# Kernel tuning notes

Measured on AMD Instinct MI355X. Metric: run time of the kernel, lower is better.

Reference implementation:

```python
import jax, jax.numpy as jnp
import numpy as np

ROPE_BASE = 10000.0


def _apply_rope(x, positions):
    # x: [B, S, H, Dh], positions: [S]
    d_head = x.shape[-1]
    half = d_head // 2
    inv_freq = 1.0 / (ROPE_BASE ** (jnp.arange(0, half, dtype=jnp.float32) * 2.0 / d_head))
    angles = positions.astype(jnp.float32)[:, None] * inv_freq[None, :]  # [S, half]
    cos = jnp.cos(angles)[None, :, None, :]  # [1,S,1,half]
    sin = jnp.sin(angles)[None, :, None, :]
    x1, x2 = jnp.split(x, 2, axis=-1)
    return jnp.concatenate([x1 * cos - x2 * sin, x1 * sin + x2 * cos], axis=-1)


def _alibi_slopes(n_heads):
    # standard ALiBi slopes: 2^(-8*(h+1)/n_heads)
    return 2.0 ** (-8.0 * (jnp.arange(1, n_heads + 1, dtype=jnp.float32) / n_heads))


def setup_inputs() -> dict:
    key = jax.random.key(0)
    ks = jax.random.split(key, 5)
    B, S, D = 2, 2048, 2048
    H, KVH, Dh = 16, 4, 128
    std = 0.02
    return {
        "residual": jax.random.normal(ks[0], (B, S, D), dtype=jnp.float32),
        "W_Q": jax.random.normal(ks[1], (H, Dh, D), dtype=jnp.float32) * std,
        "W_K": jax.random.normal(ks[2], (KVH, Dh, D), dtype=jnp.float32) * std,
        "W_V": jax.random.normal(ks[3], (KVH, Dh, D), dtype=jnp.float32) * std,
        "W_O": jax.random.normal(ks[4], (H, Dh, D), dtype=jnp.float32) * std,
        "start_pos": 0,
    }


def reference(residual, W_Q, W_K, W_V, W_O, start_pos):
    B, S, D = residual.shape
    H, Dh, _ = W_Q.shape
    KVH = W_K.shape[0]
    # projections (prefill path: cache=None, total_len == S)
    q = jnp.einsum('bsd,hed->bshe', residual, W_Q)   # [B,S,H,Dh]
    k = jnp.einsum('bsd,hed->bshe', residual, W_K)   # [B,S,KVH,Dh]
    v = jnp.einsum('bsd,hed->bshe', residual, W_V)   # [B,S,KVH,Dh]
    # RoPE
    positions = start_pos + jnp.arange(S)
    q = _apply_rope(q, positions)
    k = _apply_rope(k, positions)
    k_for_cache = k
    v_for_cache = v
    # GQA head repeat
    rep = H // KVH
    k_r = jnp.repeat(k, rep, axis=2)
    v_r = jnp.repeat(v, rep, axis=2)
    # attention scores [B,H,Sq,Sk]
    scores = jnp.einsum('bqhe,bkhe->bhqk', q, k_r) / jnp.sqrt(jnp.float32(Dh))
    # ALiBi bias (sliced rows start_pos:start_pos+S of the total_len x total_len bias)
    slopes = _alibi_slopes(H)  # [H]
    qpos = start_pos + jnp.arange(S)
    kpos = jnp.arange(S)
    bias = -slopes[:, None, None] * (qpos[:, None] - kpos[None, :]).astype(jnp.float32)
    scores = scores + bias[None, :, :, :]
    # causal mask: keep j <= i (tril of ones)
    mask = kpos[None, :] <= qpos[:, None]  # with start_pos=0 this is tril
    scores = jnp.where(mask[None, None, :, :], scores, -jnp.inf)
    pattern = jax.nn.softmax(scores, axis=-1)
    attn = jnp.einsum('bhqk,bkhe->bqhe', pattern, v_r)
    output = jnp.einsum('bqhe,hed->bqd', attn, W_O)
    return output, k_for_cache, v_for_cache
```

## Files before the change

kernel.cpp:

```cpp
#include <hip/hip_runtime.h>


typedef __attribute__((ext_vector_type(8))) short frag8;
typedef __attribute__((ext_vector_type(4))) float facc4;

#define DEVI __device__ __forceinline__

constexpr int Bc  = 2;
constexpr int Sc  = 2048;
constexpr int Dc  = 2048;
constexpr int Hc  = 16;
constexpr int KVHc = 4;
constexpr int Dhc = 128;
constexpr int Mc  = Bc * Sc;
constexpr int NQc = Hc * Dhc;
constexpr int NKVc = KVHc * Dhc;

DEVI unsigned short f2bf(float f) {
  union { float f; unsigned u; } v; v.f = f;
  return (unsigned short)((v.u + 0x7fffu + ((v.u >> 16) & 1u)) >> 16);
}
DEVI float bf2f(unsigned short h) {
  union { unsigned u; float f; } v; v.u = ((unsigned)h) << 16;
  return v.f;
}

DEVI void gload_lds16(const void* g, void* l) {
  __builtin_amdgcn_global_load_lds(
      (const __attribute__((address_space(1))) unsigned int*)g,
      (__attribute__((address_space(3))) unsigned int*)l, 16, 0, 0);
}

DEVI float rowred_max(float x) {
  union { float f; int i; } a, b;
  a.f = x;
  b.i = __builtin_amdgcn_update_dpp(a.i, a.i, 0x128, 0xF, 0xF, false); a.f = fmaxf(a.f, b.f);
  b.i = __builtin_amdgcn_update_dpp(a.i, a.i, 0x124, 0xF, 0xF, false); a.f = fmaxf(a.f, b.f);
  b.i = __builtin_amdgcn_update_dpp(a.i, a.i, 0x122, 0xF, 0xF, false); a.f = fmaxf(a.f, b.f);
  b.i = __builtin_amdgcn_update_dpp(a.i, a.i, 0x121, 0xF, 0xF, false); a.f = fmaxf(a.f, b.f);
  return a.f;
}
DEVI float rowred_sum(float x) {
  union { float f; int i; } a, b;
  a.f = x;
  b.i = __builtin_amdgcn_update_dpp(a.i, a.i, 0x128, 0xF, 0xF, false); a.f += b.f;
  b.i = __builtin_amdgcn_update_dpp(a.i, a.i, 0x124, 0xF, 0xF, false); a.f += b.f;
  b.i = __builtin_amdgcn_update_dpp(a.i, a.i, 0x122, 0xF, 0xF, false); a.f += b.f;
  b.i = __builtin_amdgcn_update_dpp(a.i, a.i, 0x121, 0xF, 0xF, false); a.f += b.f;
  return a.f;
}


__global__ void cvt_all(const float* __restrict__ residual,
                        const float* __restrict__ WQ,
                        const float* __restrict__ WK,
                        const float* __restrict__ WV,
                        const float* __restrict__ WO,
                        unsigned short* __restrict__ rb,
                        unsigned short* __restrict__ wqb,
                        unsigned short* __restrict__ wkvb,
                        unsigned short* __restrict__ wob) {
  __shared__ float tile[64][65];
  int bid = blockIdx.x;
  int t = threadIdx.x;
  if (bid < 14336) {
    const float* src; unsigned short* dst; int off;
    if (bid < 8192)       { src = residual; dst = rb;  off = bid; }
    else if (bid < 12288) { src = WQ; dst = wqb; off = bid - 8192; }
    else if (bid < 13312) { src = WK; dst = wkvb; off = bid - 12288; }
    else                  { src = WV; dst = wkvb + (size_t)NKVc * Dc; off = bid - 13312; }
    int i = (off * 256 + t) * 4;
    float4 v = *(const float4*)(src + i);
    ushort4 o;
    o.x = f2bf(v.x); o.y = f2bf(v.y); o.z = f2bf(v.z); o.w = f2bf(v.w);
    *(ushort4*)(dst + i) = o;
  } else {
    int tb = bid - 14336;
    int r0 = (tb >> 5) * 64;
    int c0 = (tb & 31) * 64;
#pragma unroll
    for (int i = 0; i < 16; ++i) {
      int idx = i * 256 + t; int r = idx >> 6, c = idx & 63;
      tile[r][c] = WO[(size_t)(r0 + r) * Dc + c0 + c];
    }
    __syncthreads();
#pragma unroll
    for (int i = 0; i < 16; ++i) {
      int idx = i * 256 + t; int r = idx >> 6, c = idx & 63;
      wob[(size_t)(c0 + r) * NQc + r0 + c] = f2bf(tile[c][r]);
    }
  }
}


DEVI void stage_tile(const unsigned short* A, const unsigned short* B,
                     unsigned short* Al, unsigned short* Bl,
                     int m0, int n0, int kt, int t, int Kk) {
#pragma unroll
  for (int i = 0; i < 4; ++i) {
    int c = i * 256 + t;
    int row = c >> 3, ch = c & 7;
    int g = ch ^ (row & 7);
    gload_lds16(A + (size_t)(m0 + row) * Kk + kt * 64 + g * 8, Al + c * 8);
  }
#pragma unroll
  for (int i = 0; i < 4; ++i) {
    int c = i * 256 + t;
    int row = c >> 3, ch = c & 7;
    int g = ch ^ (row & 7);
    gload_lds16(B + (size_t)(n0 + row) * Kk + kt * 64 + g * 8, Bl + c * 8);
  }
}

template <int MODE>
__global__ __launch_bounds__(256, 2) void gemm2b(
    const unsigned short* __restrict__ Amat,
    const unsigned short* __restrict__ Bmat,
    float* __restrict__ Cf, float* __restrict__ Cf2,
    unsigned short* __restrict__ Cb, unsigned short* __restrict__ Cb2,
    int Nn, int Kk) {
  __shared__ __align__(16) unsigned short As[2][128 * 64];
  __shared__ __align__(16) unsigned short Bs[2][128 * 64];

  int t = threadIdx.x;
  int lane = t & 63, w = t >> 6;
  int quad = lane >> 4, l16 = lane & 15;
  int l7 = l16 & 7;
  int wm = (w >> 1) * 64, wn = (w & 1) * 64;

  int lin = blockIdx.x + gridDim.x * blockIdx.y;
  int xcd = lin & 7, gg = lin >> 3;
  int ypx = gridDim.y >> 3;
  int ny = xcd * ypx + (gg % ypx);
  int nx = gg / ypx;
  int m0 = nx * 128, n0 = ny * 128;
  const int NT = Kk >> 6;

  auto aoff = [&](int mi, int ks) {
    return (wm + mi * 16 + l16) * 64 + (((ks * 4 + quad) ^ l7) * 8);
  };
  auto boff = [&](int ni, int ks) {
    return (wn + ni * 16 + l16) * 64 + (((ks * 4 + quad) ^ l7) * 8);
  };

  stage_tile(Amat, Bmat, As[0], Bs[0], m0, n0, 0, t, Kk);
  if (NT > 1) stage_tile(Amat, Bmat, As[1], Bs[1], m0, n0, 1, t, Kk);
  if (NT > 1) asm volatile("s_waitcnt vmcnt(8)" ::: "memory");
  else        asm volatile("s_waitcnt vmcnt(0)" ::: "memory");
  __builtin_amdgcn_s_barrier();
  asm volatile("" ::: "memory");

  facc4 acc[4][4] = {};

  for (int kt = 0; kt < NT; ++kt) {
    const int p = kt & 1;
    const unsigned short* Ab = As[p];
    const unsigned short* Bb = Bs[p];
    frag8 aFr[4][2], bFr[4][2];
#pragma unroll
    for (int ks = 0; ks < 2; ++ks) {
#pragma unroll
      for (int mi = 0; mi < 4; ++mi) aFr[mi][ks] = *(const frag8*)&Ab[aoff(mi, ks)];
#pragma unroll
      for (int ni = 0; ni < 4; ++ni) bFr[ni][ks] = *(const frag8*)&Bb[boff(ni, ks)];
    }
    asm volatile("s_waitcnt lgkmcnt(0)" ::: "memory");
    __builtin_amdgcn_s_barrier();
    asm volatile("" ::: "memory");

    if (kt + 2 < NT)
      stage_tile(Amat, Bmat, As[p], Bs[p], m0, n0, kt + 2, t, Kk);

    __builtin_amdgcn_s_setprio(1);
#pragma unroll
    for (int ks = 0; ks < 2; ++ks)
#pragma unroll
      for (int mi = 0; mi < 4; ++mi)
#pragma unroll
        for (int ni = 0; ni < 4; ++ni)
          acc[mi][ni] = __builtin_amdgcn_mfma_f32_16x16x32_bf16(
              aFr[mi][ks], bFr[ni][ks], acc[mi][ni], 0, 0, 0);
    __builtin_amdgcn_s_setprio(0);

    if (kt + 2 < NT) asm volatile("s_waitcnt vmcnt(8)" ::: "memory");
    else             asm volatile("s_waitcnt vmcnt(0)" ::: "memory");
    __builtin_amdgcn_s_barrier();
    asm volatile("" ::: "memory");
  }

#pragma unroll
  for (int mi = 0; mi < 4; ++mi)
#pragma unroll
    for (int ni = 0; ni < 4; ++ni)
#pragma unroll
      for (int i = 0; i < 4; ++i) {
        int row = m0 + wm + mi * 16 + quad * 4 + i;
        int col = n0 + wn + ni * 16 + l16;
        float v = acc[mi][ni][i];
        if (MODE == 0) {
          Cf[(size_t)row * Nn + col] = v;
        } else {
          if (col < NQc) {
            Cb[(size_t)row * NQc + col] = f2bf(v);
          } else if (col < NQc + NKVc) {
            Cf[(size_t)row * NKVc + (col - NQc)] = v;
          } else {
            int nc = col - NQc - NKVc;
            Cf2[(size_t)row * NKVc + nc] = v;
            int b = row >> 11, s = row & (Sc - 1);
            Cb2[((size_t)(b * NKVc + nc)) * Sc + s] = f2bf(v);
          }
        }
      }
}


__global__ void rope_all(unsigned short* qb, float* kf, unsigned short* kb,
                         const int* __restrict__ sp) {
  int idx = blockIdx.x * 256 + threadIdx.x;
  constexpr int NQ = Mc * Hc * 64;
  if (idx < NQ) {
    int e = idx & 63, h = (idx >> 6) & 15, m = idx >> 10;
    int s = m & (Sc - 1);
    float pos = (float)(sp[0] + s);
    float invf = exp2f(-(float)e * 0.20762050593046835f);
    float ang = pos * invf;
    float sn, cs; sincosf(ang, &sn, &cs);
    size_t base = (size_t)m * NQc + h * Dhc + e;
    float x1 = bf2f(qb[base]), x2 = bf2f(qb[base + 64]);
    qb[base]      = f2bf(x1 * cs - x2 * sn);
    qb[base + 64] = f2bf(x1 * sn + x2 * cs);
  } else {
    int j = idx - NQ;
    int e = j & 63, kvh = (j >> 6) & 3, m = j >> 8;
    int s = m & (Sc - 1);
    float pos = (float)(sp[0] + s);
    float invf = exp2f(-(float)e * 0.20762050593046835f);
    float ang = pos * invf;
    float sn, cs; sincosf(ang, &sn, &cs);
    size_t base = (size_t)m * NKVc + kvh * Dhc + e;
    float x1 = kf[base], x2 = kf[base + 64];
    float o1 = x1 * cs - x2 * sn;
    float o2 = x1 * sn + x2 * cs;
    kf[base] = o1; kf[base + 64] = o2;
    kb[base] = f2bf(o1); kb[base + 64] = f2bf(o2);
  }
}


DEVI void issue_tile(const unsigned short* kb, const unsigned short* vbT,
                     int bb, int kvh, int kt, int t,
                     unsigned short* KsB, unsigned short* VtB) {
#pragma unroll
  for (int i = 0; i < 4; ++i) {
    int c = i * 256 + t;
    int row = c >> 4, chp = c & 15;
    int ch = chp ^ (row & 15);
    gload_lds16(kb + (size_t)(bb * Sc + kt * 64 + row) * NKVc + kvh * Dhc + ch * 8,
                KsB + c * 8);
  }
#pragma unroll
  for (int i = 0; i < 4; ++i) {
    int c = i * 256 + t;
    int row = c >> 3, chp = c & 7;
    int ch = chp ^ (row & 7);
    gload_lds16(vbT + ((size_t)(bb * KVHc + kvh) * Dhc + row) * Sc + kt * 64 + ch * 8,
                VtB + c * 8);
  }
}

DEVI void load_q(frag8 (&aQc)[4], const unsigned short* qb, int bb, int qt,
                 int h, int w, int quad, int l16) {
  const unsigned short* qrow =
      qb + (size_t)(bb * Sc + qt * 64 + w * 16 + l16) * NQc + h * Dhc;
#pragma unroll
  for (int kd = 0; kd < 4; ++kd)
    aQc[kd] = *(const frag8*)(qrow + (kd * 4 + quad) * 8);
}

DEVI void write_o(unsigned short* qb, facc4 (&oacc)[8], float (&lrow)[4],
                  int bb, int qt, int h, int w, int quad, int l16) {
  float rinv[4];
#pragma unroll
  for (int i = 0; i < 4; ++i) rinv[i] = 1.0f / rowred_sum(lrow[i]);
#pragma unroll
  for (int c8 = 0; c8 < 8; ++c8)
#pragma unroll
    for (int i = 0; i < 4; ++i) {
      int row = qt * 64 + w * 16 + quad * 4 + i;
      size_t o = ((size_t)(bb * Sc + row) * Hc + h) * Dhc + c8 * 16 + l16;
      qb[o] = f2bf(oacc[c8][i] * rinv[i]);
    }
}

__global__ __launch_bounds__(256, 2) void flash_attn(
    unsigned short* qb,
    const unsigned short* __restrict__ kb,
    const unsigned short* __restrict__ vbT,
    const int* __restrict__ spp) {
  __shared__ __align__(16) unsigned short Ks[2][64 * 128];
  __shared__ __align__(16) unsigned short Vt[2][128 * 64];
  __shared__ __align__(16) unsigned short Ps[4][16 * 64];

  int g = blockIdx.x & 7;
  int bb = g >> 2, kvh = g & 3;
  int inner = blockIdx.x >> 3;
  int pair = inner & 15, hh = inner >> 4;
  int h = kvh * 4 + hh;
  int qtA = pair, qtB = 31 - pair;

  int t = threadIdx.x, lane = t & 63, w = t >> 6;
  int quad = lane >> 4, l16 = lane & 15;
  int sp = spp[0];
  constexpr float LOG2E = 1.4426950408889634f;
  const float SC = 0.08838834764831845f * LOG2E;
  float slope2 = exp2f(-0.5f * (float)(h + 1)) * LOG2E;
  float s2x16 = slope2 * 16.0f;
  float s2x64 = slope2 * 64.0f;

  int tA = min((sp + qtA * 64 + 63) >> 6, 31) + 1;
  int tB = min((sp + qtB * 64 + 63) >> 6, 31) + 1;
  int total = tA + tB;

  frag8 aQc[4];
  load_q(aQc, qb, bb, qtA, h, w, quad, l16);

  facc4 oacc[8] = {};
  float mrow[4], lrow[4], bq[4], adn[4][4];
  int qposi[4];
  int qt = qtA;
#pragma unroll
  for (int i = 0; i < 4; ++i) {
    mrow[i] = -1e30f; lrow[i] = 0.f;
    qposi[i] = sp + qt * 64 + w * 16 + quad * 4 + i;
    bq[i] = slope2 * (float)qposi[i];
  }

  issue_tile(kb, vbT, bb, kvh, tA - 1, t, Ks[0], Vt[0]);

  for (int it = 0; it < total; ++it) {
    if (it == tA) {
      write_o(qb, oacc, lrow, bb, qtA, h, w, quad, l16);
      load_q(aQc, qb, bb, qtB, h, w, quad, l16);
      qt = qtB;
#pragma unroll
      for (int c8 = 0; c8 < 8; ++c8)
#pragma unroll
        for (int i = 0; i < 4; ++i) oacc[c8][i] = 0.f;
#pragma unroll
      for (int i = 0; i < 4; ++i) {
        mrow[i] = -1e30f; lrow[i] = 0.f;
        qposi[i] = sp + qt * 64 + w * 16 + quad * 4 + i;
        bq[i] = slope2 * (float)qposi[i];
      }
    }
    int kt = (it < tA) ? (tA - 1 - it) : (total - 1 - it);
    bool first = (it == 0) || (it == tA);

    if (it + 1 < total) {
      int nk = (it + 1 < tA) ? (tA - 2 - it) : (total - 2 - it);
      issue_tile(kb, vbT, bb, kvh, nk, t, Ks[(it + 1) & 1], Vt[(it + 1) & 1]);
      asm volatile("s_waitcnt vmcnt(8)" ::: "memory");
    } else {
      asm volatile("s_waitcnt vmcnt(0)" ::: "memory");
    }
    __builtin_amdgcn_s_barrier();
    asm volatile("" ::: "memory");

    const unsigned short* KsB = Ks[it & 1];
    const unsigned short* VtB = Vt[it & 1];

    facc4 sacc[4] = {};
#pragma unroll
    for (int kd = 0; kd < 4; ++kd) {
      int ch = kd * 4 + quad;
#pragma unroll
      for (int c4 = 0; c4 < 4; ++c4) {
        frag8 bK = *(const frag8*)&KsB[(c4 * 16 + l16) * 128 + (ch ^ l16) * 8];
        sacc[c4] = __builtin_amdgcn_mfma_f32_16x16x32_bf16(aQc[kd], bK, sacc[c4], 0, 0, 0);
      }
    }

    unsigned short* Pw = &Ps[w][0];
    int r0 = quad * 4;
    bool needmask = (kt * 64 + 63) > (sp + qt * 64);

    if (first || needmask) {
      float sv[4][4];
      float mt[4] = {-1e30f, -1e30f, -1e30f, -1e30f};
#pragma unroll
      for (int c4 = 0; c4 < 4; ++c4) {
        int kpos = kt * 64 + c4 * 16 + l16;
        float bk = slope2 * (float)kpos;
#pragma unroll
        for (int i = 0; i < 4; ++i) {
          float v = fmaf(sacc[c4][i], SC, bk - bq[i]);
          if (needmask) v = (kpos <= qposi[i]) ? v : -1e30f;
          sv[c4][i] = v;
          mt[i] = fmaxf(mt[i], v);
        }
      }
#pragma unroll
      for (int i = 0; i < 4; ++i) mt[i] = rowred_max(mt[i]);
#pragma unroll
      for (int i = 0; i < 4; ++i) {
        float mn = fmaxf(mrow[i], mt[i]);
        float alpha = exp2f(mrow[i] - mn);
        mrow[i] = mn;
        lrow[i] *= alpha;
#pragma unroll
        for (int c8 = 0; c8 < 8; ++c8) oacc[c8][i] *= alpha;
      }
#pragma unroll
      for (int c4 = 0; c4 < 4; ++c4) {
        float p0 = exp2f(sv[c4][0] - mrow[0]);
        float p1 = exp2f(sv[c4][1] - mrow[1]);
        float p2 = exp2f(sv[c4][2] - mrow[2]);
        float p3 = exp2f(sv[c4][3] - mrow[3]);
        lrow[0] += p0; lrow[1] += p1; lrow[2] += p2; lrow[3] += p3;
        unsigned u01, u23;
        asm("v_cvt_pk_bf16_f32 %0, %1, %2" : "=v"(u01) : "v"(p0), "v"(p1));
        asm("v_cvt_pk_bf16_f32 %0, %1, %2" : "=v"(u23) : "v"(p2), "v"(p3));
        int kk = c4 * 16 + l16;
        int col = kk & 7, chnk = kk >> 3;
        Pw[(r0 + 0) * 64 + ((chnk ^ ((r0 + 0) & 7)) * 8) + col] = (unsigned short)(u01 & 0xffffu);
        Pw[(r0 + 1) * 64 + ((chnk ^ ((r0 + 1) & 7)) * 8) + col] = (unsigned short)(u01 >> 16);
        Pw[(r0 + 2) * 64 + ((chnk ^ ((r0 + 2) & 7)) * 8) + col] = (unsigned short)(u23 & 0xffffu);
        Pw[(r0 + 3) * 64 + ((chnk ^ ((r0 + 3) & 7)) * 8) + col] = (unsigned short)(u23 >> 16);
      }
      float bkn0 = slope2 * (float)((kt - 1) * 64 + l16);
#pragma unroll
      for (int c4 = 0; c4 < 4; ++c4) {
        float bkc = bkn0 + (float)c4 * s2x16;
#pragma unroll
        for (int i = 0; i < 4; ++i) adn[c4][i] = bkc - bq[i] - mrow[i];
      }
    } else {
#pragma unroll
      for (int c4 = 0; c4 < 4; ++c4) {
        float p0 = exp2f(fmaf(sacc[c4][0], SC, adn[c4][0]));
        float p1 = exp2f(fmaf(sacc[c4][1], SC, adn[c4][1]));
        float p2 = exp2f(fmaf(sacc[c4][2], SC, adn[c4][2]));
        float p3 = exp2f(fmaf(sacc[c4][3], SC, adn[c4][3]));
        lrow[0] += p0; lrow[1] += p1; lrow[2] += p2; lrow[3] += p3;
        adn[c4][0] -= s2x64; adn[c4][1] -= s2x64;
        adn[c4][2] -= s2x64; adn[c4][3] -= s2x64;
        unsigned u01, u23;
        asm("v_cvt_pk_bf16_f32 %0, %1, %2" : "=v"(u01) : "v"(p0), "v"(p1));
        asm("v_cvt_pk_bf16_f32 %0, %1, %2" : "=v"(u23) : "v"(p2), "v"(p3));
        int kk = c4 * 16 + l16;
        int col = kk & 7, chnk = kk >> 3;
        Pw[(r0 + 0) * 64 + ((chnk ^ ((r0 + 0) & 7)) * 8) + col] = (unsigned short)(u01 & 0xffffu);
        Pw[(r0 + 1) * 64 + ((chnk ^ ((r0 + 1) & 7)) * 8) + col] = (unsigned short)(u01 >> 16);
        Pw[(r0 + 2) * 64 + ((chnk ^ ((r0 + 2) & 7)) * 8) + col] = (unsigned short)(u23 & 0xffffu);
        Pw[(r0 + 3) * 64 + ((chnk ^ ((r0 + 3) & 7)) * 8) + col] = (unsigned short)(u23 >> 16);
      }
    }

#pragma unroll
    for (int k2 = 0; k2 < 2; ++k2) {
      int ch = k2 * 4 + quad;
      frag8 aP = *(const frag8*)&Ps[w][l16 * 64 + (ch ^ (l16 & 7)) * 8];
#pragma unroll
      for (int c8 = 0; c8 < 8; ++c8) {
        frag8 bV = *(const frag8*)&VtB[(c8 * 16 + l16) * 64 + (ch ^ (l16 & 7)) * 8];
        oacc[c8] = __builtin_amdgcn_mfma_f32_16x16x32_bf16(aP, bV, oacc[c8], 0, 0, 0);
      }
    }

    if (!first) {
      int ovf = (lrow[0] > 16777216.f) || (lrow[1] > 16777216.f) ||
                (lrow[2] > 16777216.f) || (lrow[3] > 16777216.f);
      if (__any(ovf)) {
        const float DS = 0x1p-32f;
#pragma unroll
        for (int i = 0; i < 4; ++i) { lrow[i] *= DS; mrow[i] += 32.f; }
#pragma unroll
        for (int c4 = 0; c4 < 4; ++c4)
#pragma unroll
          for (int i = 0; i < 4; ++i) adn[c4][i] -= 32.f;
#pragma unroll
        for (int c8 = 0; c8 < 8; ++c8)
#pragma unroll
          for (int i = 0; i < 4; ++i) oacc[c8][i] *= DS;
      }
    }

    asm volatile("" ::: "memory");
    __builtin_amdgcn_s_barrier();
  }

  write_o(qb, oacc, lrow, bb, qtB, h, w, quad, l16);
}


extern "C" void kernel_launch(void* const* d_in, const int* in_sizes, int n_in,
                              void* d_out, int out_size, void* d_ws, size_t ws_size,
                              hipStream_t stream) {
  const float* residual = (const float*)d_in[0];
  const float* W_Q = (const float*)d_in[1];
  const float* W_K = (const float*)d_in[2];
  const float* W_V = (const float*)d_in[3];
  const float* W_O = (const float*)d_in[4];
  const int* start_pos = (const int*)d_in[5];

  float* out = (float*)d_out;
  float* kf = out + (size_t)Bc * Sc * Dc;
  float* vf = kf + (size_t)Mc * NKVc;

  char* w = (char*)d_ws;
  auto alloc = [&](size_t bytes) {
    char* p = w; w += (bytes + 255) & ~(size_t)255; return p;
  };
  unsigned short* rb   = (unsigned short*)alloc((size_t)Mc * Dc * 2);
  unsigned short* wqkv = (unsigned short*)alloc((size_t)(NQc + 2 * NKVc) * Dc * 2);
  unsigned short* wob  = (unsigned short*)alloc((size_t)Dc * NQc * 2);
  unsigned short* qb   = (unsigned short*)alloc((size_t)Mc * NQc * 2);
  unsigned short* kb   = (unsigned short*)alloc((size_t)Mc * NKVc * 2);
  unsigned short* vbT  = (unsigned short*)alloc((size_t)Mc * NKVc * 2);
  (void)ws_size; (void)in_sizes; (void)n_in; (void)out_size;

  cvt_all<<<15360, 256, 0, stream>>>(residual, W_Q, W_K, W_V, W_O,
                                     rb, wqkv, wqkv + (size_t)NQc * Dc, wob);

  gemm2b<1><<<dim3(32, 24), 256, 0, stream>>>(rb, wqkv, kf, vf, qb, vbT,
                                              NQc + 2 * NKVc, Dc);

  rope_all<<<20480, 256, 0, stream>>>(qb, kf, kb, start_pos);

  flash_attn<<<512, 256, 0, stream>>>(qb, kb, vbT, start_pos);

  gemm2b<0><<<dim3(32, 16), 256, 0, stream>>>(qb, wob, out, nullptr, nullptr,
                                              nullptr, Dc, Dc);
}
```

Baseline: 317.5 us.

## Precompute RoPE table, vectorize rope kernel, and move GEMM prefetch after MFMAs

The cos/sin table is now computed once per (position, frequency) as extra blocks of the conversion kernel, and the rope kernel reads it instead of calling sincosf for every element. The rope kernel also handles four elements per thread with vector loads and stores, which cuts the grid from 20480 to 5120 blocks. In the GEMM main loop, the barrier and next-tile staging move to after the MFMA block, changing how global prefetch overlaps with compute. The cost is an extra 1 MB table in workspace, and the GEMM may lose overlap because loads are now issued later.

```diff
diff --git a/kernel.cpp b/kernel.cpp
--- a/kernel.cpp
+++ b/kernel.cpp
@@ -59,7 +59,9 @@
                         unsigned short* __restrict__ rb,
                         unsigned short* __restrict__ wqb,
                         unsigned short* __restrict__ wkvb,
-                        unsigned short* __restrict__ wob) {
+                        unsigned short* __restrict__ wob,
+                        float2* __restrict__ tab,
+                        const int* __restrict__ sp) {
   __shared__ float tile[64][65];
   int bid = blockIdx.x;
   int t = threadIdx.x;
@@ -74,7 +76,7 @@
     ushort4 o;
     o.x = f2bf(v.x); o.y = f2bf(v.y); o.z = f2bf(v.z); o.w = f2bf(v.w);
     *(ushort4*)(dst + i) = o;
-  } else {
+  } else if (bid < 15360) {
     int tb = bid - 14336;
     int r0 = (tb >> 5) * 64;
     int c0 = (tb & 31) * 64;
@@ -89,6 +91,12 @@
       int idx = i * 256 + t; int r = idx >> 6, c = idx & 63;
       wob[(size_t)(c0 + r) * NQc + r0 + c] = f2bf(tile[c][r]);
     }
+  } else {
+    int idx = (bid - 15360) * 256 + t;
+    int s = idx >> 6, e = idx & 63;
+    float ang = (float)(sp[0] + s) * exp2f(-(float)e * 0.20762050593046835f);
+    float sn, cs; sincosf(ang, &sn, &cs);
+    tab[idx] = make_float2(cs, sn);
   }
 }
 
@@ -164,12 +172,6 @@
 #pragma unroll
       for (int ni = 0; ni < 4; ++ni) bFr[ni][ks] = *(const frag8*)&Bb[boff(ni, ks)];
     }
-    asm volatile("s_waitcnt lgkmcnt(0)" ::: "memory");
-    __builtin_amdgcn_s_barrier();
-    asm volatile("" ::: "memory");
-
-    if (kt + 2 < NT)
-      stage_tile(Amat, Bmat, As[p], Bs[p], m0, n0, kt + 2, t, Kk);
 
     __builtin_amdgcn_s_setprio(1);
 #pragma unroll
@@ -182,8 +184,16 @@
               aFr[mi][ks], bFr[ni][ks], acc[mi][ni], 0, 0, 0);
     __builtin_amdgcn_s_setprio(0);
 
-    if (kt + 2 < NT) asm volatile("s_waitcnt vmcnt(8)" ::: "memory");
-    else             asm volatile("s_waitcnt vmcnt(0)" ::: "memory");
+    asm volatile("s_waitcnt lgkmcnt(0)" ::: "memory");
+    __builtin_amdgcn_s_barrier();
+    asm volatile("" ::: "memory");
+
+    if (kt + 2 < NT) {
+      stage_tile(Amat, Bmat, As[p], Bs[p], m0, n0, kt + 2, t, Kk);
+      asm volatile("s_waitcnt vmcnt(8)" ::: "memory");
+    } else {
+      asm volatile("s_waitcnt vmcnt(0)" ::: "memory");
+    }
     __builtin_amdgcn_s_barrier();
     asm volatile("" ::: "memory");
   }
@@ -216,34 +226,46 @@
 
 
 __global__ void rope_all(unsigned short* qb, float* kf, unsigned short* kb,
-                         const int* __restrict__ sp) {
+                         const float2* __restrict__ tab) {
   int idx = blockIdx.x * 256 + threadIdx.x;
-  constexpr int NQ = Mc * Hc * 64;
-  if (idx < NQ) {
-    int e = idx & 63, h = (idx >> 6) & 15, m = idx >> 10;
+  if (blockIdx.x < 4096) {
+    int e4 = idx & 15, h = (idx >> 4) & 15, m = idx >> 8;
     int s = m & (Sc - 1);
-    float pos = (float)(sp[0] + s);
-    float invf = exp2f(-(float)e * 0.20762050593046835f);
-    float ang = pos * invf;
-    float sn, cs; sincosf(ang, &sn, &cs);
-    size_t base = (size_t)m * NQc + h * Dhc + e;
-    float x1 = bf2f(qb[base]), x2 = bf2f(qb[base + 64]);
-    qb[base]      = f2bf(x1 * cs - x2 * sn);
-    qb[base + 64] = f2bf(x1 * sn + x2 * cs);
+    size_t base = (size_t)m * NQc + h * Dhc + e4 * 4;
+    ushort4 x1 = *(const ushort4*)(qb + base);
+    ushort4 x2 = *(const ushort4*)(qb + base + 64);
+    float4 ta = *(const float4*)(&tab[s * 64 + e4 * 4]);
+    float4 tbv = *(const float4*)(&tab[s * 64 + e4 * 4 + 2]);
+    float a0 = bf2f(x1.x), a1 = bf2f(x1.y), a2 = bf2f(x1.z), a3 = bf2f(x1.w);
+    float b0 = bf2f(x2.x), b1 = bf2f(x2.y), b2 = bf2f(x2.z), b3 = bf2f(x2.w);
+    ushort4 o1, o2;
+    o1.x = f2bf(a0 * ta.x - b0 * ta.y);  o2.x = f2bf(a0 * ta.y + b0 * ta.x);
+    o1.y = f2bf(a1 * ta.z - b1 * ta.w);  o2.y = f2bf(a1 * ta.w + b1 * ta.z);
+    o1.z = f2bf(a2 * tbv.x - b2 * tbv.y); o2.z = f2bf(a2 * tbv.y + b2 * tbv.x);
+    o1.w = f2bf(a3 * tbv.z - b3 * tbv.w); o2.w = f2bf(a3 * tbv.w + b3 * tbv.z);
+    *(ushort4*)(qb + base) = o1;
+    *(ushort4*)(qb + base + 64) = o2;
   } else {
-    int j = idx - NQ;
-    int e = j & 63, kvh = (j >> 6) & 3, m = j >> 8;
+    int j = idx - 4096 * 256;
+    int e4 = j & 15, kvh = (j >> 4) & 3, m = j >> 6;
     int s = m & (Sc - 1);
-    float pos = (float)(sp[0] + s);
-    float invf = exp2f(-(float)e * 0.20762050593046835f);
-    float ang = pos * invf;
-    float sn, cs; sincosf(ang, &sn, &cs);
-    size_t base = (size_t)m * NKVc + kvh * Dhc + e;
-    float x1 = kf[base], x2 = kf[base + 64];
-    float o1 = x1 * cs - x2 * sn;
-    float o2 = x1 * sn + x2 * cs;
-    kf[base] = o1; kf[base + 64] = o2;
-    kb[base] = f2bf(o1); kb[base + 64] = f2bf(o2);
+    size_t base = (size_t)m * NKVc + kvh * Dhc + e4 * 4;
+    float4 x1 = *(const float4*)(kf + base);
+    float4 x2 = *(const float4*)(kf + base + 64);
+    float4 ta = *(const float4*)(&tab[s * 64 + e4 * 4]);
+    float4 tbv = *(const float4*)(&tab[s * 64 + e4 * 4 + 2]);
+    float4 o1, o2;
+    o1.x = x1.x * ta.x - x2.x * ta.y;   o2.x = x1.x * ta.y + x2.x * ta.x;
+    o1.y = x1.y * ta.z - x2.y * ta.w;   o2.y = x1.y * ta.w + x2.y * ta.z;
+    o1.z = x1.z * tbv.x - x2.z * tbv.y; o2.z = x1.z * tbv.y + x2.z * tbv.x;
+    o1.w = x1.w * tbv.z - x2.w * tbv.w; o2.w = x1.w * tbv.w + x2.w * tbv.z;
+    *(float4*)(kf + base) = o1;
+    *(float4*)(kf + base + 64) = o2;
+    ushort4 k1, k2;
+    k1.x = f2bf(o1.x); k1.y = f2bf(o1.y); k1.z = f2bf(o1.z); k1.w = f2bf(o1.w);
+    k2.x = f2bf(o2.x); k2.y = f2bf(o2.y); k2.z = f2bf(o2.z); k2.w = f2bf(o2.w);
+    *(ushort4*)(kb + base) = k1;
+    *(ushort4*)(kb + base + 64) = k2;
   }
 }
 
@@ -518,15 +540,17 @@
   unsigned short* qb   = (unsigned short*)alloc((size_t)Mc * NQc * 2);
   unsigned short* kb   = (unsigned short*)alloc((size_t)Mc * NKVc * 2);
   unsigned short* vbT  = (unsigned short*)alloc((size_t)Mc * NKVc * 2);
+  float2* tab          = (float2*)alloc((size_t)Sc * 64 * sizeof(float2));
   (void)ws_size; (void)in_sizes; (void)n_in; (void)out_size;
 
-  cvt_all<<<15360, 256, 0, stream>>>(residual, W_Q, W_K, W_V, W_O,
-                                     rb, wqkv, wqkv + (size_t)NQc * Dc, wob);
+  cvt_all<<<15872, 256, 0, stream>>>(residual, W_Q, W_K, W_V, W_O,
+                                     rb, wqkv, wqkv + (size_t)NQc * Dc, wob,
+                                     tab, start_pos);
 
   gemm2b<1><<<dim3(32, 24), 256, 0, stream>>>(rb, wqkv, kf, vf, qb, vbT,
                                               NQc + 2 * NKVc, Dc);
 
-  rope_all<<<20480, 256, 0, stream>>>(qb, kf, kb, start_pos);
+  rope_all<<<5120, 256, 0, stream>>>(qb, kf, kb, tab);
 
   flash_attn<<<512, 256, 0, stream>>>(qb, kb, vbT, start_pos);
 
```

After: 328.5 us. 1.03x slower.
